# Kernel tuning notes

Measured on AMD Instinct MI355X. Metric: run time of the kernel, lower is better.

## Reference

```python
import jax, jax.numpy as jnp
import numpy as np

D_MODEL = 1024
NUM_HEADS = 16
D_K = D_MODEL // NUM_HEADS
B, T = 2, 2048


def setup_inputs() -> dict:
    key = jax.random.key(0)
    ks = jax.random.split(key, 11)
    s = 1.0 / np.sqrt(D_MODEL)
    inp = {
        "q": jax.random.normal(ks[0], (B, T, D_MODEL), jnp.float32),
        "k": jax.random.normal(ks[1], (B, T, D_MODEL), jnp.float32),
        "v": jax.random.normal(ks[2], (B, T, D_MODEL), jnp.float32),
        "mask": jnp.tril(jnp.ones((1, 1, T, T), jnp.int32)),  # causal
        "wq": jax.random.normal(ks[3], (D_MODEL, D_MODEL), jnp.float32) * s,
        "bq": jnp.zeros((D_MODEL,), jnp.float32),
        "wk": jax.random.normal(ks[4], (D_MODEL, D_MODEL), jnp.float32) * s,
        "bk": jnp.zeros((D_MODEL,), jnp.float32),
        "wv": jax.random.normal(ks[5], (D_MODEL, D_MODEL), jnp.float32) * s,
        "bv": jnp.zeros((D_MODEL,), jnp.float32),
        "wo": jax.random.normal(ks[6], (D_MODEL, D_MODEL), jnp.float32) * s,
        "bo": jnp.zeros((D_MODEL,), jnp.float32),
    }
    return inp


def reference(q, k, v, mask, wq, bq, wk, bk, wv, bv, wo, bo):
    Bq, Tq, _ = q.shape
    Tk = k.shape[1]
    # projections, split into heads: (B, H, T, d_k)
    qh = (q @ wq + bq).reshape(Bq, Tq, NUM_HEADS, D_K).transpose(0, 2, 1, 3)
    kh = (k @ wk + bk).reshape(Bq, Tk, NUM_HEADS, D_K).transpose(0, 2, 1, 3)
    vh = (v @ wv + bv).reshape(Bq, Tk, NUM_HEADS, D_K).transpose(0, 2, 1, 3)
    scores = jnp.einsum("bhqd,bhkd->bhqk", qh, kh) / jnp.sqrt(jnp.float32(D_K))
    scores = jnp.where(mask == 0, jnp.float32(-1e9), scores)
    attn = jax.nn.softmax(scores, axis=-1)
    ctx = jnp.einsum("bhqk,bhkd->bhqd", attn, vh)
    ctx = ctx.transpose(0, 2, 1, 3).reshape(Bq, Tq, D_MODEL)
    return ctx @ wo + bo
```

## Files before the change

### kernel.cpp

```cpp
#include <hip/hip_runtime.h>
#include <hip/hip_bf16.h>

#define DM 1024
#define NH 16
#define DK 64
#define TT 2048
#define BATCH 2

typedef __attribute__((ext_vector_type(8))) short bf16x8;
typedef __attribute__((ext_vector_type(4))) float f32x4;
typedef __attribute__((ext_vector_type(4))) unsigned short u16x4;
typedef unsigned short u16;

__device__ inline u16 f2b(float x){ __hip_bfloat16 h = __float2bfloat16(x); return *reinterpret_cast<u16*>(&h); }

__device__ inline void gl_lds16(const u16* g, u16* l) {
  __builtin_amdgcn_global_load_lds(
      (const __attribute__((address_space(1))) unsigned int*)g,
      (__attribute__((address_space(3))) unsigned int*)l, 16, 0, 0);
}

__global__ __launch_bounds__(256) void prep(const float* __restrict__ q, const float* __restrict__ k,
                                            const float* __restrict__ v,
                                            const float* __restrict__ wq, const float* __restrict__ wk,
                                            const float* __restrict__ wv, const float* __restrict__ wo,
                                            u16* __restrict__ qb, u16* __restrict__ kb,
                                            u16* __restrict__ vb, u16* __restrict__ wt) {
  int z = blockIdx.z;
  if (z < 3) {
    const float* src = z==0 ? q : z==1 ? k : v;
    u16* dst = z==0 ? qb : z==1 ? kb : vb;
    size_t i = ((size_t)blockIdx.x*256 + threadIdx.x)*8;
    f32x4 a = *(const f32x4*)(src+i);
    f32x4 b = *(const f32x4*)(src+i+4);
    union { bf16x8 v8; u16 e[8]; } u;
    #pragma unroll
    for (int j=0;j<4;j++){ u.e[j] = f2b(a[j]); u.e[4+j] = f2b(b[j]); }
    *(bf16x8*)(dst+i) = u.v8;
  } else {
    int bx = blockIdx.x;
    if (bx >= 1024) return;
    __shared__ float tile[32][33];
    const float* src = z==3 ? wq : z==4 ? wk : z==5 ? wv : wo;
    u16* dst = wt + (size_t)(z-3)*DM*DM;
    int bxx = bx & 31, byy = bx >> 5;
    int tx = threadIdx.x & 31, ty = threadIdx.x >> 5;
    int x  = bxx*32 + tx;
    int y0 = byy*32 + ty;
    #pragma unroll
    for (int i=0;i<32;i+=8) tile[ty+i][tx] = src[(size_t)(y0+i)*DM + x];
    __syncthreads();
    int xo = byy*32 + tx;
    int yo = bxx*32 + ty;
    #pragma unroll
    for (int i=0;i<32;i+=8) dst[(size_t)(yo+i)*DM + xo] = f2b(tile[tx][ty+i]);
  }
}

__global__ __launch_bounds__(512, 2) void gemm_qkv(const u16* __restrict__ qb, const u16* __restrict__ kb,
                                                   const u16* __restrict__ vb, const u16* __restrict__ wt,
                                                   const float* __restrict__ bq, const float* __restrict__ bk,
                                                   const float* __restrict__ bv,
                                                   u16* __restrict__ qh, u16* __restrict__ kh,
                                                   u16* __restrict__ vhT) {
  const int bid = blockIdx.x;
  const int swz = (bid & 7)*24 + (bid >> 3);
  const int z  = swz >> 6;
  const int rb = swz & 63;
  const int row0 = (rb >> 2) * 256;
  const int col0 = (rb & 3) * 256;

  const u16* A = z==0 ? qb : z==1 ? kb : vb;
  const u16* W = wt + (size_t)z*DM*DM;
  const float* bias = z==0 ? bq : z==1 ? bk : bv;
  u16* outv = z==0 ? qh : z==1 ? kh : vhT;
  const int mode = (z==2);
  const float oscale = (z==0) ? 0.125f : 1.0f;

  __shared__ __align__(16) u16 As[2][16384];
  __shared__ __align__(16) u16 Bs[2][16384];

  const int tid = threadIdx.x, lane = tid & 63, wid = tid >> 6;
  const int li = lane & 15, quad = lane >> 4, l7 = lane & 7;
  const int wr = wid >> 2, wc = wid & 3;

  int r_[2], gs_[2];
  #pragma unroll
  for (int c=0;c<2;c++){ int idx = tid + c*512; int rr = idx>>3; int gd = idx&7; r_[c]=rr; gs_[c]=gd^(rr&7); }

  auto stage = [&](int op, int t, int hf, int slot){
    const u16* base = op ? W : A;
    const int rowbase = (op ? col0 : row0) + hf*128;
    u16* lb = (op ? Bs[slot] : As[slot]) + hf*8192;
    #pragma unroll
    for (int c=0;c<2;c++){
      gl_lds16(base + (size_t)(rowbase + r_[c])*DM + t*64 + gs_[c]*8,
               lb + ((wid*64 + c*512) << 3));
    }
  };

  f32x4 acc[8][4];
  #pragma unroll
  for (int i=0;i<8;i++)
    #pragma unroll
    for (int j=0;j<4;j++) acc[i][j] = f32x4{0.f,0.f,0.f,0.f};

  stage(1, 0, 0, 0); stage(1, 0, 1, 0);
  stage(0, 0, 0, 0); stage(0, 0, 1, 0);
  stage(1, 1, 0, 1); stage(1, 1, 1, 1);
  asm volatile("s_waitcnt vmcnt(4)" ::: "memory");
  __builtin_amdgcn_s_barrier();

  bf16x8 b[4][2];
  for (int i = 0; i < 8; i++) {
    const int t2 = 2*i;
    #pragma unroll
    for (int half = 0; half < 2; half++) {
      const int slot = half;
      #pragma unroll
      for (int q = 0; q < 4; q++) {
        if (q == 0) {
          const u16* bb = Bs[slot] + (wc>>1)*8192 + (wc&1)*4096;
          #pragma unroll
          for (int c=0;c<4;c++)
            #pragma unroll
            for (int kh=0;kh<2;kh++)
              b[c][kh] = *(const bf16x8*)&bb[(c*16 + li)*64 + ((quad + 4*kh) ^ l7)*8];
        }
        bf16x8 a[2][2];
        {
          const u16* ab = As[slot] + wr*8192;
          #pragma unroll
          for (int rr2=0; rr2<2; rr2++)
            #pragma unroll
            for (int kh=0;kh<2;kh++)
              a[rr2][kh] = *(const bf16x8*)&ab[((q*2+rr2)*16 + li)*64 + ((quad + 4*kh) ^ l7)*8];
        }
        {
          const int sop = (q >= 2);
          const int st  = t2 + 1 + half + (q >= 2);
          const int shf = q & 1;
          const int ssl = (q >= 2) ? half : (1 - half);
          if (st <= 15) stage(sop, st, shf, ssl);
        }
        if (q == 0) asm volatile("s_waitcnt lgkmcnt(8)" ::: "memory");
        __builtin_amdgcn_s_barrier();
        asm volatile("s_waitcnt lgkmcnt(0)" ::: "memory");
        __builtin_amdgcn_sched_barrier(0);
        __builtin_amdgcn_s_setprio(1);
        #pragma unroll
        for (int rr2=0; rr2<2; rr2++)
          #pragma unroll
          for (int c=0;c<4;c++)
            #pragma unroll
            for (int kh=0;kh<2;kh++)
              acc[q*2+rr2][c] = __builtin_amdgcn_mfma_f32_16x16x32_bf16(a[rr2][kh], b[c][kh], acc[q*2+rr2][c], 0,0,0);
        __builtin_amdgcn_s_setprio(0);
        if (q == 3) {
          if (half == 0) {
            if (i < 7) asm volatile("s_waitcnt vmcnt(4)" ::: "memory");
            else       asm volatile("s_waitcnt vmcnt(0)" ::: "memory");
          } else {
            if (i < 7) asm volatile("s_waitcnt vmcnt(4)" ::: "memory");
          }
        }
        __builtin_amdgcn_s_barrier();
      }
    }
  }

  if (!mode) {
    #pragma unroll
    for (int c=0;c<4;c++) {
      int col = col0 + wc*64 + c*16 + li;
      float bsv = bias[col];
      #pragma unroll
      for (int fr=0; fr<8; fr++) {
        int rowb = row0 + wr*128 + fr*16 + quad*4;
        #pragma unroll
        for (int r=0;r<4;r++)
          outv[(size_t)(rowb + r)*DM + col] = f2b((acc[fr][c][r] + bsv) * oscale);
      }
    }
  } else {
    #pragma unroll
    for (int c=0;c<4;c++) {
      int col = col0 + wc*64 + c*16 + li;
      float bsv = bias[col];
      int hh = col >> 6, d = col & 63;
      #pragma unroll
      for (int fr=0; fr<8; fr++) {
        int rowb = row0 + wr*128 + fr*16 + quad*4;
        int bb = rowb >> 11, t0 = rowb & (TT-1);
        u16x4 w;
        #pragma unroll
        for (int r=0;r<4;r++) w[r] = f2b(acc[fr][c][r] + bsv);
        *(u16x4*)&outv[(((size_t)(bb*NH + hh)*DK + d)*TT) + t0] = w;
      }
    }
  }
}

__global__ __launch_bounds__(256) void gemm_out64(const u16* __restrict__ A, const u16* __restrict__ W,
                                                  const float* __restrict__ bias, float* __restrict__ out) {
  __shared__ __align__(16) u16 As[3][128*32];
  __shared__ __align__(16) u16 Bs[3][64*32];
  const int tid = threadIdx.x, lane = tid & 63, wid = tid >> 6;
  const int li = lane & 15, quad = lane >> 4;
  const int row0 = blockIdx.x*128, col0 = blockIdx.y*64;
  const int wr = wid & 1, wc = wid >> 1;

  const int srow = lane >> 2;
  const int scol = ((lane & 3) ^ ((srow >> 1) & 3)) * 8;
  const int rsw  = (li >> 1) & 3;

  auto stage = [&](int hh, int bufi) {
    const int kk = hh*32;
    #pragma unroll
    for (int c=0;c<2;c++) {
      int ch = wid*2 + c;
      gl_lds16(A + (size_t)(row0 + ch*16 + srow)*DM + kk + scol, &As[bufi][ch*512]);
    }
    gl_lds16(W + (size_t)(col0 + wid*16 + srow)*DM + kk + scol, &Bs[bufi][wid*512]);
  };

  f32x4 acc[4][2];
  #pragma unroll
  for (int i=0;i<4;i++)
    #pragma unroll
    for (int j=0;j<2;j++) acc[i][j] = f32x4{0.f,0.f,0.f,0.f};

  stage(0, 0);
  stage(1, 1);
  asm volatile("s_waitcnt vmcnt(3)" ::: "memory");
  __builtin_amdgcn_s_barrier();

  int buf = 0;
  for (int h = 0; h < 32; h++) {
    bf16x8 a[4], b[2];
    #pragma unroll
    for (int i=0;i<4;i++) a[i] = *(const bf16x8*)&As[buf][(wr*64 + i*16 + li)*32 + (quad ^ rsw)*8];
    #pragma unroll
    for (int j=0;j<2;j++) b[j] = *(const bf16x8*)&Bs[buf][(wc*32 + j*16 + li)*32 + (quad ^ rsw)*8];

    if (h < 30) { int nb = buf + 2; if (nb >= 3) nb -= 3; stage(h+2, nb); }

    __builtin_amdgcn_s_setprio(1);
    #pragma unroll
    for (int i=0;i<4;i++)
      #pragma unroll
      for (int j=0;j<2;j++)
        acc[i][j] = __builtin_amdgcn_mfma_f32_16x16x32_bf16(a[i], b[j], acc[i][j], 0,0,0);
    __builtin_amdgcn_s_setprio(0);

    if (h < 30)       asm volatile("s_waitcnt vmcnt(3)" ::: "memory");
    else if (h == 30) asm volatile("s_waitcnt vmcnt(0)" ::: "memory");
    __builtin_amdgcn_s_barrier();
    if (++buf == 3) buf = 0;
  }

  #pragma unroll
  for (int j=0;j<2;j++) {
    int col = col0 + wc*32 + j*16 + li;
    float bsv = bias[col];
    #pragma unroll
    for (int i=0;i<4;i++) {
      #pragma unroll
      for (int r=0;r<4;r++) {
        int row = row0 + wr*64 + i*16 + quad*4 + r;
        out[(size_t)row*DM + col] = acc[i][j][r] + bsv;
      }
    }
  }
}

__global__ __launch_bounds__(256) void flash(const u16* __restrict__ qh, const u16* __restrict__ kh,
                                             const u16* __restrict__ vhT, u16* __restrict__ ctx) {
  const int bh = blockIdx.x;
  const int y  = blockIdx.y;
  const int qt = (y < 8) ? (15 - y) : (y - 8);
  const int b = bh >> 4, h = bh & 15;
  const u16* Q  = qh  + (size_t)b*TT*DM + h*DK;
  const u16* K  = kh  + (size_t)b*TT*DM + h*DK;
  const u16* Vt = vhT + (size_t)bh*DK*TT;

  const int tid = threadIdx.x, lane = tid & 63, wid = tid >> 6;
  const int li = lane & 15, quad = lane >> 4, l7 = lane & 7;

  __shared__ __align__(16) u16 Kl[2][64][64];
  __shared__ __align__(16) u16 Vl[2][64][64];
  __shared__ __align__(16) u16 Pb[4][16][64];

  const int sr = tid >> 3;
  const int sg = tid & 7;
  const int ssl = (sg ^ (sr & 7)) * 8;

  const int nt  = 2*qt + 2;
  const int qw0 = qt*128 + wid*32;

  bf16x8 qf[2][2];
  #pragma unroll
  for (int su=0; su<2; su++)
    #pragma unroll
    for (int k2=0; k2<2; k2++)
      qf[su][k2] = *(const bf16x8*)&Q[(size_t)(qw0 + su*16 + li)*DM + k2*32 + quad*8];

  f32x4 o[2][4];
  #pragma unroll
  for (int su=0; su<2; su++)
    #pragma unroll
    for (int d=0; d<4; d++) o[su][d] = f32x4{0.f,0.f,0.f,0.f};
  float lp[2] = {0.f, 0.f};

  bf16x8 kr0 = *(const bf16x8*)&K[(size_t)(sr   )*DM + sg*8];
  bf16x8 kr1 = *(const bf16x8*)&K[(size_t)(sr+32)*DM + sg*8];
  bf16x8 vr0 = *(const bf16x8*)&Vt[(size_t)(sr   )*TT + sg*8];
  bf16x8 vr1 = *(const bf16x8*)&Vt[(size_t)(sr+32)*TT + sg*8];

  for (int it = 0; it < nt; it++) {
    const int k0 = it*64;
    const int s = it & 1;
    *(bf16x8*)&Kl[s][sr   ][ssl] = kr0;
    *(bf16x8*)&Kl[s][sr+32][ssl] = kr1;
    *(bf16x8*)&Vl[s][sr   ][ssl] = vr0;
    *(bf16x8*)&Vl[s][sr+32][ssl] = vr1;
    __syncthreads();
    if (it+1 < nt) {
      const int k1 = k0 + 64;
      kr0 = *(const bf16x8*)&K[(size_t)(k1+sr   )*DM + sg*8];
      kr1 = *(const bf16x8*)&K[(size_t)(k1+sr+32)*DM + sg*8];
      vr0 = *(const bf16x8*)&Vt[(size_t)(sr   )*TT + k1 + sg*8];
      vr1 = *(const bf16x8*)&Vt[(size_t)(sr+32)*TT + k1 + sg*8];
    }

    if (k0 <= qw0 + 31) {
      f32x4 sacc[2][4];
      __builtin_amdgcn_s_setprio(1);
      #pragma unroll
      for (int c=0;c<4;c++) {
        bf16x8 kf0 = *(const bf16x8*)&Kl[s][c*16+li][((quad    ) ^ l7)*8];
        bf16x8 kf1 = *(const bf16x8*)&Kl[s][c*16+li][((quad + 4) ^ l7)*8];
        #pragma unroll
        for (int su=0; su<2; su++) {
          f32x4 t = __builtin_amdgcn_mfma_f32_16x16x32_bf16(kf0, qf[su][0], f32x4{0.f,0.f,0.f,0.f}, 0,0,0);
          sacc[su][c] = __builtin_amdgcn_mfma_f32_16x16x32_bf16(kf1, qf[su][1], t, 0,0,0);
        }
      }
      __builtin_amdgcn_s_setprio(0);

      bf16x8 vf[4][2];
      #pragma unroll
      for (int d=0; d<4; d++) {
        vf[d][0] = *(const bf16x8*)&Vl[s][d*16+li][((quad    ) ^ l7)*8];
        vf[d][1] = *(const bf16x8*)&Vl[s][d*16+li][((quad + 4) ^ l7)*8];
      }

      #pragma unroll
      for (int su=0; su<2; su++) {
        const int qr = qw0 + su*16;
        if (k0 <= qr + 15) {
          const int qq = qr + li;
          float p[4][4];
          if (k0 + 63 > qr) {
            #pragma unroll
            for (int c=0;c<4;c++)
              #pragma unroll
              for (int r=0;r<4;r++){
                int key = k0 + c*16 + quad*4 + r;
                p[c][r] = (key <= qq) ? __expf(sacc[su][c][r]) : 0.f;
              }
          } else {
            #pragma unroll
            for (int c=0;c<4;c++)
              #pragma unroll
              for (int r=0;r<4;r++)
                p[c][r] = __expf(sacc[su][c][r]);
          }
          #pragma unroll
          for (int c=0;c<4;c++)
            #pragma unroll
            for (int r=0;r<4;r++)
              lp[su] += p[c][r];

          #pragma unroll
          for (int c=0;c<4;c++) {
            u16x4 w;
            #pragma unroll
            for (int r=0;r<4;r++) w[r] = f2b(p[c][r]);
            const int gc = c*2 + (quad>>1);
            *(u16x4*)&Pb[wid][li][((gc ^ l7)*8) + (quad&1)*4] = w;
          }
          __builtin_amdgcn_wave_barrier();
          __asm__ __volatile__("s_waitcnt lgkmcnt(0)");
          bf16x8 pf0 = *(const bf16x8*)&Pb[wid][li][((quad    ) ^ l7)*8];
          bf16x8 pf1 = *(const bf16x8*)&Pb[wid][li][((quad + 4) ^ l7)*8];

          __builtin_amdgcn_s_setprio(1);
          #pragma unroll
          for (int d=0;d<4;d++){
            o[su][d] = __builtin_amdgcn_mfma_f32_16x16x32_bf16(vf[d][0], pf0, o[su][d], 0,0,0);
            o[su][d] = __builtin_amdgcn_mfma_f32_16x16x32_bf16(vf[d][1], pf1, o[su][d], 0,0,0);
          }
          __builtin_amdgcn_s_setprio(0);
        }
      }
    }
  }

  #pragma unroll
  for (int su=0; su<2; su++) {
    float lpv = lp[su];
    lpv += __shfl_xor(lpv, 16, 64);
    lpv += __shfl_xor(lpv, 32, 64);
    float rl = 1.0f / lpv;
    const int qq = qw0 + su*16 + li;
    #pragma unroll
    for (int d=0;d<4;d++){
      u16x4 w;
      #pragma unroll
      for (int r=0;r<4;r++) w[r] = f2b(o[su][d][r] * rl);
      *(u16x4*)&ctx[(size_t)(b*TT + qq)*DM + h*DK + d*16 + quad*4] = w;
    }
  }
}

extern "C" void kernel_launch(void* const* d_in, const int* in_sizes, int n_in,
                              void* d_out, int out_size, void* d_ws, size_t ws_size,
                              hipStream_t stream) {
  const float* q   = (const float*)d_in[0];
  const float* k   = (const float*)d_in[1];
  const float* v   = (const float*)d_in[2];
  const float* wq  = (const float*)d_in[4];
  const float* bq  = (const float*)d_in[5];
  const float* wk  = (const float*)d_in[6];
  const float* bk  = (const float*)d_in[7];
  const float* wv  = (const float*)d_in[8];
  const float* bv  = (const float*)d_in[9];
  const float* wo  = (const float*)d_in[10];
  const float* bo  = (const float*)d_in[11];
  float* out = (float*)d_out;

  const size_t SZ = (size_t)BATCH*TT*DM;
  u16* wt  = (u16*)d_ws;
  u16* qb  = wt + (size_t)4*DM*DM;
  u16* kb  = qb + SZ;
  u16* vb  = kb + SZ;
  u16* qh  = vb + SZ;
  u16* kh  = qh + SZ;
  u16* vhT = kh + SZ;
  u16* ctx = qb;

  prep<<<dim3(2048, 1, 7), 256, 0, stream>>>(q, k, v, wq, wk, wv, wo, qb, kb, vb, wt);

  gemm_qkv<<<dim3(192, 1, 1), 512, 0, stream>>>(qb, kb, vb, wt, bq, bk, bv, qh, kh, vhT);

  flash<<<dim3(BATCH*NH, 16), 256, 0, stream>>>(qh, kh, vhT, ctx);

  gemm_out64<<<dim3(4096/128, DM/64), 256, 0, stream>>>(ctx, wt + (size_t)3*DM*DM, bo, out);
}
```

Measured before the change: 225.1 us.

## Split flash attention key range across two wave groups and fold log2e into Q scale

The flash kernel now runs 512 threads per block. Two groups of four waves each process half of the causal key range for the same query tile, and their unnormalized outputs and row sums are merged through shared memory at the end. This shortens the serial key loop per block and adds parallelism on a grid with few blocks. Separately, the Q scale now includes log2(e), so exp2f can replace __expf. The cost is more LDS use, an extra reduction step, and imbalance because only group 0 writes the output.

```diff
diff --git a/kernel.cpp b/kernel.cpp
--- a/kernel.cpp
+++ b/kernel.cpp
@@ -75,7 +75,7 @@
   const float* bias = z==0 ? bq : z==1 ? bk : bv;
   u16* outv = z==0 ? qh : z==1 ? kh : vhT;
   const int mode = (z==2);
-  const float oscale = (z==0) ? 0.125f : 1.0f;
+  const float oscale = (z==0) ? 0.18033688f : 1.0f;
 
   __shared__ __align__(16) u16 As[2][16384];
   __shared__ __align__(16) u16 Bs[2][16384];
@@ -274,8 +274,8 @@
   }
 }
 
-__global__ __launch_bounds__(256) void flash(const u16* __restrict__ qh, const u16* __restrict__ kh,
-                                             const u16* __restrict__ vhT, u16* __restrict__ ctx) {
+__global__ __launch_bounds__(512, 4) void flash(const u16* __restrict__ qh, const u16* __restrict__ kh,
+                                                const u16* __restrict__ vhT, u16* __restrict__ ctx) {
   const int bh = blockIdx.x;
   const int y  = blockIdx.y;
   const int qt = (y < 8) ? (15 - y) : (y - 8);
@@ -285,18 +285,21 @@
   const u16* Vt = vhT + (size_t)bh*DK*TT;
 
   const int tid = threadIdx.x, lane = tid & 63, wid = tid >> 6;
+  const int kg = wid >> 2;
+  const int w  = wid & 3;
   const int li = lane & 15, quad = lane >> 4, l7 = lane & 7;
 
-  __shared__ __align__(16) u16 Kl[2][64][64];
-  __shared__ __align__(16) u16 Vl[2][64][64];
-  __shared__ __align__(16) u16 Pb[4][16][64];
-
-  const int sr = tid >> 3;
-  const int sg = tid & 7;
+  __shared__ __align__(16) u16 KVs[2][2][2][4096];
+  __shared__ __align__(16) u16 Pb[8][16][64];
+
+  const int H = qt + 1;
+  const int kbase = kg * H * 64;
+  const int qw0 = qt*128 + w*32;
+
+  const int t2 = tid & 255;
+  const int sr = t2 >> 3;
+  const int sg = t2 & 7;
   const int ssl = (sg ^ (sr & 7)) * 8;
-
-  const int nt  = 2*qt + 2;
-  const int qw0 = qt*128 + wid*32;
 
   bf16x8 qf[2][2];
   #pragma unroll
@@ -312,20 +315,20 @@
     for (int d=0; d<4; d++) o[su][d] = f32x4{0.f,0.f,0.f,0.f};
   float lp[2] = {0.f, 0.f};
 
-  bf16x8 kr0 = *(const bf16x8*)&K[(size_t)(sr   )*DM + sg*8];
-  bf16x8 kr1 = *(const bf16x8*)&K[(size_t)(sr+32)*DM + sg*8];
-  bf16x8 vr0 = *(const bf16x8*)&Vt[(size_t)(sr   )*TT + sg*8];
-  bf16x8 vr1 = *(const bf16x8*)&Vt[(size_t)(sr+32)*TT + sg*8];
-
-  for (int it = 0; it < nt; it++) {
-    const int k0 = it*64;
-    const int s = it & 1;
-    *(bf16x8*)&Kl[s][sr   ][ssl] = kr0;
-    *(bf16x8*)&Kl[s][sr+32][ssl] = kr1;
-    *(bf16x8*)&Vl[s][sr   ][ssl] = vr0;
-    *(bf16x8*)&Vl[s][sr+32][ssl] = vr1;
+  bf16x8 kr0 = *(const bf16x8*)&K[(size_t)(kbase+sr   )*DM + sg*8];
+  bf16x8 kr1 = *(const bf16x8*)&K[(size_t)(kbase+sr+32)*DM + sg*8];
+  bf16x8 vr0 = *(const bf16x8*)&Vt[(size_t)(sr   )*TT + kbase + sg*8];
+  bf16x8 vr1 = *(const bf16x8*)&Vt[(size_t)(sr+32)*TT + kbase + sg*8];
+
+  for (int itl = 0; itl < H; itl++) {
+    const int k0 = kbase + itl*64;
+    const int s = itl & 1;
+    *(bf16x8*)&KVs[kg][0][s][(sr   )*64 + ssl] = kr0;
+    *(bf16x8*)&KVs[kg][0][s][(sr+32)*64 + ssl] = kr1;
+    *(bf16x8*)&KVs[kg][1][s][(sr   )*64 + ssl] = vr0;
+    *(bf16x8*)&KVs[kg][1][s][(sr+32)*64 + ssl] = vr1;
     __syncthreads();
-    if (it+1 < nt) {
+    if (itl+1 < H) {
       const int k1 = k0 + 64;
       kr0 = *(const bf16x8*)&K[(size_t)(k1+sr   )*DM + sg*8];
       kr1 = *(const bf16x8*)&K[(size_t)(k1+sr+32)*DM + sg*8];
@@ -334,12 +337,14 @@
     }
 
     if (k0 <= qw0 + 31) {
+      const u16* Klp = &KVs[kg][0][s][0];
+      const u16* Vlp = &KVs[kg][1][s][0];
       f32x4 sacc[2][4];
       __builtin_amdgcn_s_setprio(1);
       #pragma unroll
       for (int c=0;c<4;c++) {
-        bf16x8 kf0 = *(const bf16x8*)&Kl[s][c*16+li][((quad    ) ^ l7)*8];
-        bf16x8 kf1 = *(const bf16x8*)&Kl[s][c*16+li][((quad + 4) ^ l7)*8];
+        bf16x8 kf0 = *(const bf16x8*)&Klp[(c*16+li)*64 + ((quad    ) ^ l7)*8];
+        bf16x8 kf1 = *(const bf16x8*)&Klp[(c*16+li)*64 + ((quad + 4) ^ l7)*8];
         #pragma unroll
         for (int su=0; su<2; su++) {
           f32x4 t = __builtin_amdgcn_mfma_f32_16x16x32_bf16(kf0, qf[su][0], f32x4{0.f,0.f,0.f,0.f}, 0,0,0);
@@ -351,8 +356,8 @@
       bf16x8 vf[4][2];
       #pragma unroll
       for (int d=0; d<4; d++) {
-        vf[d][0] = *(const bf16x8*)&Vl[s][d*16+li][((quad    ) ^ l7)*8];
-        vf[d][1] = *(const bf16x8*)&Vl[s][d*16+li][((quad + 4) ^ l7)*8];
+        vf[d][0] = *(const bf16x8*)&Vlp[(d*16+li)*64 + ((quad    ) ^ l7)*8];
+        vf[d][1] = *(const bf16x8*)&Vlp[(d*16+li)*64 + ((quad + 4) ^ l7)*8];
       }
 
       #pragma unroll
@@ -367,14 +372,14 @@
               #pragma unroll
               for (int r=0;r<4;r++){
                 int key = k0 + c*16 + quad*4 + r;
-                p[c][r] = (key <= qq) ? __expf(sacc[su][c][r]) : 0.f;
+                p[c][r] = (key <= qq) ? exp2f(sacc[su][c][r]) : 0.f;
               }
           } else {
             #pragma unroll
             for (int c=0;c<4;c++)
               #pragma unroll
               for (int r=0;r<4;r++)
-                p[c][r] = __expf(sacc[su][c][r]);
+                p[c][r] = exp2f(sacc[su][c][r]);
           }
           #pragma unroll
           for (int c=0;c<4;c++)
@@ -384,11 +389,11 @@
 
           #pragma unroll
           for (int c=0;c<4;c++) {
-            u16x4 w;
-            #pragma unroll
-            for (int r=0;r<4;r++) w[r] = f2b(p[c][r]);
+            u16x4 wv;
+            #pragma unroll
+            for (int r=0;r<4;r++) wv[r] = f2b(p[c][r]);
             const int gc = c*2 + (quad>>1);
-            *(u16x4*)&Pb[wid][li][((gc ^ l7)*8) + (quad&1)*4] = w;
+            *(u16x4*)&Pb[wid][li][((gc ^ l7)*8) + (quad&1)*4] = wv;
           }
           __builtin_amdgcn_wave_barrier();
           __asm__ __volatile__("s_waitcnt lgkmcnt(0)");
@@ -407,19 +412,40 @@
     }
   }
 
-  #pragma unroll
-  for (int su=0; su<2; su++) {
-    float lpv = lp[su];
-    lpv += __shfl_xor(lpv, 16, 64);
-    lpv += __shfl_xor(lpv, 32, 64);
-    float rl = 1.0f / lpv;
-    const int qq = qw0 + su*16 + li;
-    #pragma unroll
-    for (int d=0;d<4;d++){
-      u16x4 w;
-      #pragma unroll
-      for (int r=0;r<4;r++) w[r] = f2b(o[su][d][r] * rl);
-      *(u16x4*)&ctx[(size_t)(b*TT + qq)*DM + h*DK + d*16 + quad*4] = w;
+  __syncthreads();
+  float* ex = (float*)&KVs[0][0][0][0];
+  const int xo = (w*64 + lane)*36;
+  if (kg == 1) {
+    #pragma unroll
+    for (int su=0; su<2; su++)
+      #pragma unroll
+      for (int d=0; d<4; d++)
+        *(f32x4*)&ex[xo + su*16 + d*4] = o[su][d];
+    ex[xo+32] = lp[0]; ex[xo+33] = lp[1];
+  }
+  __syncthreads();
+  if (kg == 0) {
+    #pragma unroll
+    for (int su=0; su<2; su++)
+      #pragma unroll
+      for (int d=0; d<4; d++)
+        o[su][d] += *(const f32x4*)&ex[xo + su*16 + d*4];
+    lp[0] += ex[xo+32]; lp[1] += ex[xo+33];
+
+    #pragma unroll
+    for (int su=0; su<2; su++) {
+      float lpv = lp[su];
+      lpv += __shfl_xor(lpv, 16, 64);
+      lpv += __shfl_xor(lpv, 32, 64);
+      float rl = 1.0f / lpv;
+      const int qq = qw0 + su*16 + li;
+      #pragma unroll
+      for (int d=0;d<4;d++){
+        u16x4 wv;
+        #pragma unroll
+        for (int r=0;r<4;r++) wv[r] = f2b(o[su][d][r] * rl);
+        *(u16x4*)&ctx[(size_t)(b*TT + qq)*DM + h*DK + d*16 + quad*4] = wv;
+      }
     }
   }
 }
@@ -454,7 +480,7 @@
 
   gemm_qkv<<<dim3(192, 1, 1), 512, 0, stream>>>(qb, kb, vb, wt, bq, bk, bv, qh, kh, vhT);
 
-  flash<<<dim3(BATCH*NH, 16), 256, 0, stream>>>(qh, kh, vhT, ctx);
+  flash<<<dim3(BATCH*NH, 16), 512, 0, stream>>>(qh, kh, vhT, ctx);
 
   gemm_out64<<<dim3(4096/128, DM/64), 256, 0, stream>>>(ctx, wt + (size_t)3*DM*DM, bo, out);
 }
```

Measured after the change: 340.4 us. +51.2%, slower.

## Software-pipeline flash attention PV across iterations with triple-buffered K/V

Applied to the files above, without the earlier changes.

Restructures the flash kernel so the P·V MFMAs for tile n-1 are issued in iteration n, overlapping them with the QK^T MFMAs and softmax of the current tile, using a three-slot K/V LDS ring. It folds log2(e) into the Q scale so exp2f replaces __expf, and computes the row-sum with an MFMA against a ones vector instead of scalar adds and shuffles. It also adds an occupancy hint of 2 blocks per CU. The costs are more LDS, extra registers for the carried P fragments, and bf16 rounding of P inside the row sum.

```diff
diff --git a/kernel.cpp b/kernel.cpp
--- a/kernel.cpp
+++ b/kernel.cpp
@@ -75,7 +75,7 @@
   const float* bias = z==0 ? bq : z==1 ? bk : bv;
   u16* outv = z==0 ? qh : z==1 ? kh : vhT;
   const int mode = (z==2);
-  const float oscale = (z==0) ? 0.125f : 1.0f;
+  const float oscale = (z==0) ? 0.18033688f : 1.0f;
 
   __shared__ __align__(16) u16 As[2][16384];
   __shared__ __align__(16) u16 Bs[2][16384];
@@ -274,8 +274,8 @@
   }
 }
 
-__global__ __launch_bounds__(256) void flash(const u16* __restrict__ qh, const u16* __restrict__ kh,
-                                             const u16* __restrict__ vhT, u16* __restrict__ ctx) {
+__global__ __launch_bounds__(256, 2) void flash(const u16* __restrict__ qh, const u16* __restrict__ kh,
+                                                const u16* __restrict__ vhT, u16* __restrict__ ctx) {
   const int bh = blockIdx.x;
   const int y  = blockIdx.y;
   const int qt = (y < 8) ? (15 - y) : (y - 8);
@@ -287,8 +287,8 @@
   const int tid = threadIdx.x, lane = tid & 63, wid = tid >> 6;
   const int li = lane & 15, quad = lane >> 4, l7 = lane & 7;
 
-  __shared__ __align__(16) u16 Kl[2][64][64];
-  __shared__ __align__(16) u16 Vl[2][64][64];
+  __shared__ __align__(16) u16 Ks[3][4096];
+  __shared__ __align__(16) u16 Vs[3][4096];
   __shared__ __align__(16) u16 Pb[4][16][64];
 
   const int sr = tid >> 3;
@@ -305,41 +305,64 @@
     for (int k2=0; k2<2; k2++)
       qf[su][k2] = *(const bf16x8*)&Q[(size_t)(qw0 + su*16 + li)*DM + k2*32 + quad*8];
 
+  bf16x8 vone;
+  #pragma unroll
+  for (int j=0;j<8;j++) vone[j] = (short)0x3F80;
+
   f32x4 o[2][4];
   #pragma unroll
   for (int su=0; su<2; su++)
     #pragma unroll
     for (int d=0; d<4; d++) o[su][d] = f32x4{0.f,0.f,0.f,0.f};
-  float lp[2] = {0.f, 0.f};
+  f32x4 lpacc[2];
+  lpacc[0] = f32x4{0.f,0.f,0.f,0.f};
+  lpacc[1] = f32x4{0.f,0.f,0.f,0.f};
+
+  bf16x8 pf[2][2];
+  bool pa0 = false, pa1 = false;
 
   bf16x8 kr0 = *(const bf16x8*)&K[(size_t)(sr   )*DM + sg*8];
   bf16x8 kr1 = *(const bf16x8*)&K[(size_t)(sr+32)*DM + sg*8];
   bf16x8 vr0 = *(const bf16x8*)&Vt[(size_t)(sr   )*TT + sg*8];
   bf16x8 vr1 = *(const bf16x8*)&Vt[(size_t)(sr+32)*TT + sg*8];
-
-  for (int it = 0; it < nt; it++) {
-    const int k0 = it*64;
-    const int s = it & 1;
-    *(bf16x8*)&Kl[s][sr   ][ssl] = kr0;
-    *(bf16x8*)&Kl[s][sr+32][ssl] = kr1;
-    *(bf16x8*)&Vl[s][sr   ][ssl] = vr0;
-    *(bf16x8*)&Vl[s][sr+32][ssl] = vr1;
-    __syncthreads();
-    if (it+1 < nt) {
-      const int k1 = k0 + 64;
-      kr0 = *(const bf16x8*)&K[(size_t)(k1+sr   )*DM + sg*8];
-      kr1 = *(const bf16x8*)&K[(size_t)(k1+sr+32)*DM + sg*8];
-      vr0 = *(const bf16x8*)&Vt[(size_t)(sr   )*TT + k1 + sg*8];
-      vr1 = *(const bf16x8*)&Vt[(size_t)(sr+32)*TT + k1 + sg*8];
-    }
-
-    if (k0 <= qw0 + 31) {
-      f32x4 sacc[2][4];
+  *(bf16x8*)&Ks[0][(sr   )*64 + ssl] = kr0;
+  *(bf16x8*)&Ks[0][(sr+32)*64 + ssl] = kr1;
+  *(bf16x8*)&Vs[0][(sr   )*64 + ssl] = vr0;
+  *(bf16x8*)&Vs[0][(sr+32)*64 + ssl] = vr1;
+  kr0 = *(const bf16x8*)&K[(size_t)(64+sr   )*DM + sg*8];
+  kr1 = *(const bf16x8*)&K[(size_t)(64+sr+32)*DM + sg*8];
+  vr0 = *(const bf16x8*)&Vt[(size_t)(sr   )*TT + 64 + sg*8];
+  vr1 = *(const bf16x8*)&Vt[(size_t)(sr+32)*TT + 64 + sg*8];
+  __syncthreads();
+
+  for (int n = 0; n < nt; n++) {
+    if (n > 0) __syncthreads();
+    const int sc = n % 3;
+    if (n+1 < nt) {
+      const int sn = (n+1) % 3;
+      *(bf16x8*)&Ks[sn][(sr   )*64 + ssl] = kr0;
+      *(bf16x8*)&Ks[sn][(sr+32)*64 + ssl] = kr1;
+      *(bf16x8*)&Vs[sn][(sr   )*64 + ssl] = vr0;
+      *(bf16x8*)&Vs[sn][(sr+32)*64 + ssl] = vr1;
+    }
+    if (n+2 < nt) {
+      const int k2 = (n+2)*64;
+      kr0 = *(const bf16x8*)&K[(size_t)(k2+sr   )*DM + sg*8];
+      kr1 = *(const bf16x8*)&K[(size_t)(k2+sr+32)*DM + sg*8];
+      vr0 = *(const bf16x8*)&Vt[(size_t)(sr   )*TT + k2 + sg*8];
+      vr1 = *(const bf16x8*)&Vt[(size_t)(sr+32)*TT + k2 + sg*8];
+    }
+
+    const int k0 = n*64;
+    const bool act = (k0 <= qw0 + 31);
+
+    f32x4 sacc[2][4];
+    if (act) {
       __builtin_amdgcn_s_setprio(1);
       #pragma unroll
       for (int c=0;c<4;c++) {
-        bf16x8 kf0 = *(const bf16x8*)&Kl[s][c*16+li][((quad    ) ^ l7)*8];
-        bf16x8 kf1 = *(const bf16x8*)&Kl[s][c*16+li][((quad + 4) ^ l7)*8];
+        bf16x8 kf0 = *(const bf16x8*)&Ks[sc][(c*16+li)*64 + ((quad    ) ^ l7)*8];
+        bf16x8 kf1 = *(const bf16x8*)&Ks[sc][(c*16+li)*64 + ((quad + 4) ^ l7)*8];
         #pragma unroll
         for (int su=0; su<2; su++) {
           f32x4 t = __builtin_amdgcn_mfma_f32_16x16x32_bf16(kf0, qf[su][0], f32x4{0.f,0.f,0.f,0.f}, 0,0,0);
@@ -347,79 +370,109 @@
         }
       }
       __builtin_amdgcn_s_setprio(0);
-
+    }
+
+    if (n > 0 && (pa0 | pa1)) {
+      const int sp = (n + 2) % 3;
       bf16x8 vf[4][2];
       #pragma unroll
       for (int d=0; d<4; d++) {
-        vf[d][0] = *(const bf16x8*)&Vl[s][d*16+li][((quad    ) ^ l7)*8];
-        vf[d][1] = *(const bf16x8*)&Vl[s][d*16+li][((quad + 4) ^ l7)*8];
-      }
-
+        vf[d][0] = *(const bf16x8*)&Vs[sp][(d*16+li)*64 + ((quad    ) ^ l7)*8];
+        vf[d][1] = *(const bf16x8*)&Vs[sp][(d*16+li)*64 + ((quad + 4) ^ l7)*8];
+      }
+      if (pa0) {
+        #pragma unroll
+        for (int d=0;d<4;d++){
+          o[0][d] = __builtin_amdgcn_mfma_f32_16x16x32_bf16(vf[d][0], pf[0][0], o[0][d], 0,0,0);
+          o[0][d] = __builtin_amdgcn_mfma_f32_16x16x32_bf16(vf[d][1], pf[0][1], o[0][d], 0,0,0);
+        }
+        lpacc[0] = __builtin_amdgcn_mfma_f32_16x16x32_bf16(vone, pf[0][0], lpacc[0], 0,0,0);
+        lpacc[0] = __builtin_amdgcn_mfma_f32_16x16x32_bf16(vone, pf[0][1], lpacc[0], 0,0,0);
+      }
+      if (pa1) {
+        #pragma unroll
+        for (int d=0;d<4;d++){
+          o[1][d] = __builtin_amdgcn_mfma_f32_16x16x32_bf16(vf[d][0], pf[1][0], o[1][d], 0,0,0);
+          o[1][d] = __builtin_amdgcn_mfma_f32_16x16x32_bf16(vf[d][1], pf[1][1], o[1][d], 0,0,0);
+        }
+        lpacc[1] = __builtin_amdgcn_mfma_f32_16x16x32_bf16(vone, pf[1][0], lpacc[1], 0,0,0);
+        lpacc[1] = __builtin_amdgcn_mfma_f32_16x16x32_bf16(vone, pf[1][1], lpacc[1], 0,0,0);
+      }
+    }
+
+    if (act) {
+      const bool dg = (k0 + 63 > qw0);
       #pragma unroll
       for (int su=0; su<2; su++) {
         const int qr = qw0 + su*16;
-        if (k0 <= qr + 15) {
+        const bool sa = (k0 <= qr + 15);
+        if (sa) {
           const int qq = qr + li;
-          float p[4][4];
-          if (k0 + 63 > qr) {
-            #pragma unroll
-            for (int c=0;c<4;c++)
+          #pragma unroll
+          for (int c=0;c<4;c++) {
+            u16x4 wv;
+            if (dg) {
               #pragma unroll
               for (int r=0;r<4;r++){
                 int key = k0 + c*16 + quad*4 + r;
-                p[c][r] = (key <= qq) ? __expf(sacc[su][c][r]) : 0.f;
+                wv[r] = f2b((key <= qq) ? exp2f(sacc[su][c][r]) : 0.f);
               }
-          } else {
-            #pragma unroll
-            for (int c=0;c<4;c++)
+            } else {
               #pragma unroll
-              for (int r=0;r<4;r++)
-                p[c][r] = __expf(sacc[su][c][r]);
-          }
-          #pragma unroll
-          for (int c=0;c<4;c++)
-            #pragma unroll
-            for (int r=0;r<4;r++)
-              lp[su] += p[c][r];
-
-          #pragma unroll
-          for (int c=0;c<4;c++) {
-            u16x4 w;
-            #pragma unroll
-            for (int r=0;r<4;r++) w[r] = f2b(p[c][r]);
+              for (int r=0;r<4;r++) wv[r] = f2b(exp2f(sacc[su][c][r]));
+            }
             const int gc = c*2 + (quad>>1);
-            *(u16x4*)&Pb[wid][li][((gc ^ l7)*8) + (quad&1)*4] = w;
+            *(u16x4*)&Pb[wid][li][((gc ^ l7)*8) + (quad&1)*4] = wv;
           }
           __builtin_amdgcn_wave_barrier();
           __asm__ __volatile__("s_waitcnt lgkmcnt(0)");
-          bf16x8 pf0 = *(const bf16x8*)&Pb[wid][li][((quad    ) ^ l7)*8];
-          bf16x8 pf1 = *(const bf16x8*)&Pb[wid][li][((quad + 4) ^ l7)*8];
-
-          __builtin_amdgcn_s_setprio(1);
-          #pragma unroll
-          for (int d=0;d<4;d++){
-            o[su][d] = __builtin_amdgcn_mfma_f32_16x16x32_bf16(vf[d][0], pf0, o[su][d], 0,0,0);
-            o[su][d] = __builtin_amdgcn_mfma_f32_16x16x32_bf16(vf[d][1], pf1, o[su][d], 0,0,0);
-          }
-          __builtin_amdgcn_s_setprio(0);
-        }
-      }
+          pf[su][0] = *(const bf16x8*)&Pb[wid][li][((quad    ) ^ l7)*8];
+          pf[su][1] = *(const bf16x8*)&Pb[wid][li][((quad + 4) ^ l7)*8];
+          __asm__ __volatile__("s_waitcnt lgkmcnt(0)");
+        }
+        if (su == 0) pa0 = sa; else pa1 = sa;
+      }
+    } else { pa0 = false; pa1 = false; }
+  }
+
+  if (pa0 | pa1) {
+    const int sp = (nt + 2) % 3;
+    bf16x8 vf[4][2];
+    #pragma unroll
+    for (int d=0; d<4; d++) {
+      vf[d][0] = *(const bf16x8*)&Vs[sp][(d*16+li)*64 + ((quad    ) ^ l7)*8];
+      vf[d][1] = *(const bf16x8*)&Vs[sp][(d*16+li)*64 + ((quad + 4) ^ l7)*8];
+    }
+    if (pa0) {
+      #pragma unroll
+      for (int d=0;d<4;d++){
+        o[0][d] = __builtin_amdgcn_mfma_f32_16x16x32_bf16(vf[d][0], pf[0][0], o[0][d], 0,0,0);
+        o[0][d] = __builtin_amdgcn_mfma_f32_16x16x32_bf16(vf[d][1], pf[0][1], o[0][d], 0,0,0);
+      }
+      lpacc[0] = __builtin_amdgcn_mfma_f32_16x16x32_bf16(vone, pf[0][0], lpacc[0], 0,0,0);
+      lpacc[0] = __builtin_amdgcn_mfma_f32_16x16x32_bf16(vone, pf[0][1], lpacc[0], 0,0,0);
+    }
+    if (pa1) {
+      #pragma unroll
+      for (int d=0;d<4;d++){
+        o[1][d] = __builtin_amdgcn_mfma_f32_16x16x32_bf16(vf[d][0], pf[1][0], o[1][d], 0,0,0);
+        o[1][d] = __builtin_amdgcn_mfma_f32_16x16x32_bf16(vf[d][1], pf[1][1], o[1][d], 0,0,0);
+      }
+      lpacc[1] = __builtin_amdgcn_mfma_f32_16x16x32_bf16(vone, pf[1][0], lpacc[1], 0,0,0);
+      lpacc[1] = __builtin_amdgcn_mfma_f32_16x16x32_bf16(vone, pf[1][1], lpacc[1], 0,0,0);
     }
   }
 
   #pragma unroll
   for (int su=0; su<2; su++) {
-    float lpv = lp[su];
-    lpv += __shfl_xor(lpv, 16, 64);
-    lpv += __shfl_xor(lpv, 32, 64);
-    float rl = 1.0f / lpv;
+    float rl = 1.0f / lpacc[su][0];
     const int qq = qw0 + su*16 + li;
     #pragma unroll
     for (int d=0;d<4;d++){
-      u16x4 w;
-      #pragma unroll
-      for (int r=0;r<4;r++) w[r] = f2b(o[su][d][r] * rl);
-      *(u16x4*)&ctx[(size_t)(b*TT + qq)*DM + h*DK + d*16 + quad*4] = w;
+      u16x4 wv;
+      #pragma unroll
+      for (int r=0;r<4;r++) wv[r] = f2b(o[su][d][r] * rl);
+      *(u16x4*)&ctx[(size_t)(b*TT + qq)*DM + h*DK + d*16 + quad*4] = wv;
     }
   }
 }
```

Result: slower. 239.8 us (+6.5%).

## Load K/V fragments directly from global in flash kernel, drop LDS staging

Applied to the files above, without the earlier changes.

The flash kernel no longer stages K and V tiles through double-buffered shared memory with block-wide barriers. Each wave now reads its own MFMA fragments straight from global memory and loops only over the key tiles its causal range needs. The log2(e) factor is folded into the Q scale so exp2f can replace __expf, and launch bounds now request 4 blocks per CU. This removes the per-tile __syncthreads and shared-memory traffic, but each wave now issues redundant, less coalesced global loads for K/V and has no prefetch to hide their latency.

```diff
diff --git a/kernel.cpp b/kernel.cpp
--- a/kernel.cpp
+++ b/kernel.cpp
@@ -75,7 +75,7 @@
   const float* bias = z==0 ? bq : z==1 ? bk : bv;
   u16* outv = z==0 ? qh : z==1 ? kh : vhT;
   const int mode = (z==2);
-  const float oscale = (z==0) ? 0.125f : 1.0f;
+  const float oscale = (z==0) ? 0.18033688f : 1.0f;
 
   __shared__ __align__(16) u16 As[2][16384];
   __shared__ __align__(16) u16 Bs[2][16384];
@@ -274,8 +274,8 @@
   }
 }
 
-__global__ __launch_bounds__(256) void flash(const u16* __restrict__ qh, const u16* __restrict__ kh,
-                                             const u16* __restrict__ vhT, u16* __restrict__ ctx) {
+__global__ __launch_bounds__(256, 4) void flash(const u16* __restrict__ qh, const u16* __restrict__ kh,
+                                                const u16* __restrict__ vhT, u16* __restrict__ ctx) {
   const int bh = blockIdx.x;
   const int y  = blockIdx.y;
   const int qt = (y < 8) ? (15 - y) : (y - 8);
@@ -287,16 +287,10 @@
   const int tid = threadIdx.x, lane = tid & 63, wid = tid >> 6;
   const int li = lane & 15, quad = lane >> 4, l7 = lane & 7;
 
-  __shared__ __align__(16) u16 Kl[2][64][64];
-  __shared__ __align__(16) u16 Vl[2][64][64];
   __shared__ __align__(16) u16 Pb[4][16][64];
 
-  const int sr = tid >> 3;
-  const int sg = tid & 7;
-  const int ssl = (sg ^ (sr & 7)) * 8;
-
-  const int nt  = 2*qt + 2;
   const int qw0 = qt*128 + wid*32;
+  const int ntw = (qw0 + 31)/64 + 1;
 
   bf16x8 qf[2][2];
   #pragma unroll
@@ -312,96 +306,76 @@
     for (int d=0; d<4; d++) o[su][d] = f32x4{0.f,0.f,0.f,0.f};
   float lp[2] = {0.f, 0.f};
 
-  bf16x8 kr0 = *(const bf16x8*)&K[(size_t)(sr   )*DM + sg*8];
-  bf16x8 kr1 = *(const bf16x8*)&K[(size_t)(sr+32)*DM + sg*8];
-  bf16x8 vr0 = *(const bf16x8*)&Vt[(size_t)(sr   )*TT + sg*8];
-  bf16x8 vr1 = *(const bf16x8*)&Vt[(size_t)(sr+32)*TT + sg*8];
-
-  for (int it = 0; it < nt; it++) {
-    const int k0 = it*64;
-    const int s = it & 1;
-    *(bf16x8*)&Kl[s][sr   ][ssl] = kr0;
-    *(bf16x8*)&Kl[s][sr+32][ssl] = kr1;
-    *(bf16x8*)&Vl[s][sr   ][ssl] = vr0;
-    *(bf16x8*)&Vl[s][sr+32][ssl] = vr1;
-    __syncthreads();
-    if (it+1 < nt) {
-      const int k1 = k0 + 64;
-      kr0 = *(const bf16x8*)&K[(size_t)(k1+sr   )*DM + sg*8];
-      kr1 = *(const bf16x8*)&K[(size_t)(k1+sr+32)*DM + sg*8];
-      vr0 = *(const bf16x8*)&Vt[(size_t)(sr   )*TT + k1 + sg*8];
-      vr1 = *(const bf16x8*)&Vt[(size_t)(sr+32)*TT + k1 + sg*8];
-    }
-
-    if (k0 <= qw0 + 31) {
-      f32x4 sacc[2][4];
-      __builtin_amdgcn_s_setprio(1);
-      #pragma unroll
-      for (int c=0;c<4;c++) {
-        bf16x8 kf0 = *(const bf16x8*)&Kl[s][c*16+li][((quad    ) ^ l7)*8];
-        bf16x8 kf1 = *(const bf16x8*)&Kl[s][c*16+li][((quad + 4) ^ l7)*8];
-        #pragma unroll
-        for (int su=0; su<2; su++) {
-          f32x4 t = __builtin_amdgcn_mfma_f32_16x16x32_bf16(kf0, qf[su][0], f32x4{0.f,0.f,0.f,0.f}, 0,0,0);
-          sacc[su][c] = __builtin_amdgcn_mfma_f32_16x16x32_bf16(kf1, qf[su][1], t, 0,0,0);
-        }
-      }
-      __builtin_amdgcn_s_setprio(0);
-
-      bf16x8 vf[4][2];
-      #pragma unroll
-      for (int d=0; d<4; d++) {
-        vf[d][0] = *(const bf16x8*)&Vl[s][d*16+li][((quad    ) ^ l7)*8];
-        vf[d][1] = *(const bf16x8*)&Vl[s][d*16+li][((quad + 4) ^ l7)*8];
-      }
-
+  for (int n = 0; n < ntw; n++) {
+    const int k0 = n*64;
+
+    f32x4 sacc[2][4];
+    #pragma unroll
+    for (int c=0;c<4;c++) {
+      const u16* krow = &K[(size_t)(k0 + c*16 + li)*DM];
+      bf16x8 kf0 = *(const bf16x8*)&krow[     quad*8];
+      bf16x8 kf1 = *(const bf16x8*)&krow[32 + quad*8];
       #pragma unroll
       for (int su=0; su<2; su++) {
-        const int qr = qw0 + su*16;
-        if (k0 <= qr + 15) {
-          const int qq = qr + li;
-          float p[4][4];
-          if (k0 + 63 > qr) {
+        f32x4 t = __builtin_amdgcn_mfma_f32_16x16x32_bf16(kf0, qf[su][0], f32x4{0.f,0.f,0.f,0.f}, 0,0,0);
+        sacc[su][c] = __builtin_amdgcn_mfma_f32_16x16x32_bf16(kf1, qf[su][1], t, 0,0,0);
+      }
+    }
+
+    bf16x8 vf[4][2];
+    #pragma unroll
+    for (int d=0; d<4; d++) {
+      const u16* vrow = &Vt[(size_t)(d*16 + li)*TT + k0];
+      vf[d][0] = *(const bf16x8*)&vrow[     quad*8];
+      vf[d][1] = *(const bf16x8*)&vrow[32 + quad*8];
+    }
+
+    const bool dg = (k0 + 63 > qw0);
+    #pragma unroll
+    for (int su=0; su<2; su++) {
+      const int qr = qw0 + su*16;
+      if (k0 <= qr + 15) {
+        const int qq = qr + li;
+        float p[4][4];
+        if (dg) {
+          #pragma unroll
+          for (int c=0;c<4;c++)
             #pragma unroll
-            for (int c=0;c<4;c++)
-              #pragma unroll
-              for (int r=0;r<4;r++){
-                int key = k0 + c*16 + quad*4 + r;
-                p[c][r] = (key <= qq) ? __expf(sacc[su][c][r]) : 0.f;
-              }
-          } else {
-            #pragma unroll
-            for (int c=0;c<4;c++)
-              #pragma unroll
-              for (int r=0;r<4;r++)
-                p[c][r] = __expf(sacc[su][c][r]);
-          }
+            for (int r=0;r<4;r++){
+              int key = k0 + c*16 + quad*4 + r;
+              p[c][r] = (key <= qq) ? exp2f(sacc[su][c][r]) : 0.f;
+            }
+        } else {
           #pragma unroll
           for (int c=0;c<4;c++)
             #pragma unroll
             for (int r=0;r<4;r++)
-              lp[su] += p[c][r];
-
-          #pragma unroll
-          for (int c=0;c<4;c++) {
-            u16x4 w;
-            #pragma unroll
-            for (int r=0;r<4;r++) w[r] = f2b(p[c][r]);
-            const int gc = c*2 + (quad>>1);
-            *(u16x4*)&Pb[wid][li][((gc ^ l7)*8) + (quad&1)*4] = w;
-          }
-          __builtin_amdgcn_wave_barrier();
-          __asm__ __volatile__("s_waitcnt lgkmcnt(0)");
-          bf16x8 pf0 = *(const bf16x8*)&Pb[wid][li][((quad    ) ^ l7)*8];
-          bf16x8 pf1 = *(const bf16x8*)&Pb[wid][li][((quad + 4) ^ l7)*8];
-
-          __builtin_amdgcn_s_setprio(1);
-          #pragma unroll
-          for (int d=0;d<4;d++){
-            o[su][d] = __builtin_amdgcn_mfma_f32_16x16x32_bf16(vf[d][0], pf0, o[su][d], 0,0,0);
-            o[su][d] = __builtin_amdgcn_mfma_f32_16x16x32_bf16(vf[d][1], pf1, o[su][d], 0,0,0);
-          }
-          __builtin_amdgcn_s_setprio(0);
+              p[c][r] = exp2f(sacc[su][c][r]);
+        }
+        #pragma unroll
+        for (int c=0;c<4;c++)
+          #pragma unroll
+          for (int r=0;r<4;r++)
+            lp[su] += p[c][r];
+
+        #pragma unroll
+        for (int c=0;c<4;c++) {
+          u16x4 wv;
+          #pragma unroll
+          for (int r=0;r<4;r++) wv[r] = f2b(p[c][r]);
+          const int gc = c*2 + (quad>>1);
+          *(u16x4*)&Pb[wid][li][((gc ^ l7)*8) + (quad&1)*4] = wv;
+        }
+        __builtin_amdgcn_wave_barrier();
+        __asm__ __volatile__("s_waitcnt lgkmcnt(0)");
+        bf16x8 pf0 = *(const bf16x8*)&Pb[wid][li][((quad    ) ^ l7)*8];
+        bf16x8 pf1 = *(const bf16x8*)&Pb[wid][li][((quad + 4) ^ l7)*8];
+        __asm__ __volatile__("s_waitcnt lgkmcnt(0)");
+
+        #pragma unroll
+        for (int d=0;d<4;d++){
+          o[su][d] = __builtin_amdgcn_mfma_f32_16x16x32_bf16(vf[d][0], pf0, o[su][d], 0,0,0);
+          o[su][d] = __builtin_amdgcn_mfma_f32_16x16x32_bf16(vf[d][1], pf1, o[su][d], 0,0,0);
         }
       }
     }
@@ -416,10 +390,10 @@
     const int qq = qw0 + su*16 + li;
     #pragma unroll
     for (int d=0;d<4;d++){
-      u16x4 w;
-      #pragma unroll
-      for (int r=0;r<4;r++) w[r] = f2b(o[su][d][r] * rl);
-      *(u16x4*)&ctx[(size_t)(b*TT + qq)*DM + h*DK + d*16 + quad*4] = w;
+      u16x4 wv;
+      #pragma unroll
+      for (int r=0;r<4;r++) wv[r] = f2b(o[su][d][r] * rl);
+      *(u16x4*)&ctx[(size_t)(b*TT + qq)*DM + h*DK + d*16 + quad*4] = wv;
     }
   }
 }
```

Result: slower. 332.4 us (+47.7%).
